# Kernel optimization log

Hardware: AMD Instinct MI355X
Metric: run time of the kernel (lower is better)

## Reference

```python
import jax, jax.numpy as jnp
import numpy as np

D = 1024      # n_embd
H = 16        # n_head
HD = D // H   # head_size = 64


def _layernorm(x, g, b, eps=1e-5):
    mu = jnp.mean(x, axis=-1, keepdims=True)
    var = jnp.mean((x - mu) ** 2, axis=-1, keepdims=True)
    return (x - mu) * jax.lax.rsqrt(var + eps) * g + b


def setup_inputs() -> dict:
    key = jax.random.key(0)
    ks = jax.random.split(key, 12)
    s = lambda fan_in: 1.0 / np.sqrt(fan_in)
    inp = {
        "x": jax.random.normal(ks[0], (4, 2048, D), dtype=jnp.float32),
        # attention projections (bias=False in Head), per-head weights fused into [D, D]
        "wq": jax.random.uniform(ks[1], (D, D), jnp.float32, -s(D), s(D)),
        "wk": jax.random.uniform(ks[2], (D, D), jnp.float32, -s(D), s(D)),
        "wv": jax.random.uniform(ks[3], (D, D), jnp.float32, -s(D), s(D)),
        "wo": jax.random.uniform(ks[4], (D, D), jnp.float32, -s(D), s(D)),
        "bo": jax.random.uniform(ks[5], (D,), jnp.float32, -s(D), s(D)),
        # feed-forward: D -> 4D -> D
        "w1": jax.random.uniform(ks[6], (D, 4 * D), jnp.float32, -s(D), s(D)),
        "b1": jax.random.uniform(ks[7], (4 * D,), jnp.float32, -s(D), s(D)),
        "w2": jax.random.uniform(ks[8], (4 * D, D), jnp.float32, -s(4 * D), s(4 * D)),
        "b2": jax.random.uniform(ks[9], (D,), jnp.float32, -s(4 * D), s(4 * D)),
        # layernorms
        "g_ln1": jnp.ones((D,), jnp.float32),
        "b_ln1": jnp.zeros((D,), jnp.float32),
        "g_ln2": jnp.ones((D,), jnp.float32),
        "b_ln2": jnp.zeros((D,), jnp.float32),
    }
    return inp


def reference(x, wq, wk, wv, wo, bo, w1, b1, w2, b2, g_ln1, b_ln1, g_ln2, b_ln2):
    B, T, _ = x.shape
    # --- self-attention on ln1(x) ---
    h = _layernorm(x, g_ln1, b_ln1)
    q = (h @ wq).reshape(B, T, H, HD)
    k = (h @ wk).reshape(B, T, H, HD)
    v = (h @ wv).reshape(B, T, H, HD)
    scores = jnp.einsum("bqhd,bkhd->bhqk", q, k) * (HD ** -0.5)
    causal = jnp.tril(jnp.ones((T, T), dtype=bool))
    scores = jnp.where(causal, scores, -jnp.inf)
    wei = jax.nn.softmax(scores, axis=-1)                    # [B,H,T,T]
    attn = jnp.einsum("bhqk,bkhd->bqhd", wei, v).reshape(B, T, D)
    x = x + attn @ wo + bo
    # --- feed-forward on ln2(x) ---
    h2 = _layernorm(x, g_ln2, b_ln2)
    x = x + jax.nn.relu(h2 @ w1 + b1) @ w2 + b2
    return x
```

## Files before the change

kernel.cpp:

```cpp
#include <hip/hip_runtime.h>
#include <cstdint>

typedef __bf16 bf16x8 __attribute__((ext_vector_type(8)));
typedef float f32x4 __attribute__((ext_vector_type(4)));
typedef unsigned int u32x4 __attribute__((ext_vector_type(4)));
typedef unsigned int u32x2 __attribute__((ext_vector_type(2)));
typedef unsigned short u16x4 __attribute__((ext_vector_type(4)));

#define D_MODEL 1024
#define SEQ     2048
#define NBATCH  4
#define NHEAD   16
#define HDIM    64
#define NTOK    (NBATCH * SEQ)
#define QSCALE  0.18033688011112042f

__device__ __forceinline__ unsigned short f2bf(float f) {
  unsigned int u = __builtin_bit_cast(unsigned int, f);
  u += 0x7FFFu + ((u >> 16) & 1u);
  return (unsigned short)(u >> 16);
}

__device__ __forceinline__ float bf2f(unsigned short s) {
  return __builtin_bit_cast(float, (unsigned int)s << 16);
}

__device__ __forceinline__ bf16x8 load8bf(const unsigned short* p) {
  return __builtin_bit_cast(bf16x8, *(const u32x4*)p);
}

__device__ __forceinline__ f32x4 mfma16(bf16x8 a, bf16x8 b, f32x4 c) {
  return __builtin_amdgcn_mfma_f32_16x16x32_bf16(a, b, c, 0, 0, 0);
}

__device__ __forceinline__ void gload16(const unsigned short* g, unsigned short* l) {
  __builtin_amdgcn_global_load_lds((__attribute__((address_space(1))) void*)g,
                                   (__attribute__((address_space(3))) void*)l, 16, 0, 0);
}

__global__ __launch_bounds__(256) void tcast_all(const float* __restrict__ wq,
                                                 const float* __restrict__ wk,
                                                 const float* __restrict__ wv,
                                                 const float* __restrict__ wo,
                                                 const float* __restrict__ w1,
                                                 const float* __restrict__ w2,
                                                 unsigned short* __restrict__ wqkv_t,
                                                 unsigned short* __restrict__ wo_t,
                                                 unsigned short* __restrict__ w1_t,
                                                 unsigned short* __restrict__ w2_t) {
  const int id = blockIdx.x;
  const float* in; unsigned short* out; int K, N, k0, n0;
  if (id < 4096) {
    const int seg = id >> 10, r = id & 1023;
    in  = seg == 0 ? wq : seg == 1 ? wk : seg == 2 ? wv : wo;
    out = seg == 3 ? wo_t : wqkv_t + (size_t)seg * 1024 * 1024;
    K = 1024; N = 1024; n0 = (r & 31) * 32; k0 = (r >> 5) * 32;
  } else if (id < 8192) {
    const int r = id - 4096;
    in = w1; out = w1_t; K = 1024; N = 4096;
    n0 = (r & 127) * 32; k0 = (r >> 7) * 32;
  } else {
    const int r = id - 8192;
    in = w2; out = w2_t; K = 4096; N = 1024;
    n0 = (r & 31) * 32; k0 = (r >> 5) * 32;
  }
  __shared__ float tile[32][33];
  const int tx = threadIdx.x & 31, ty = threadIdx.x >> 5;
  #pragma unroll
  for (int j = 0; j < 4; ++j)
    tile[ty + 8 * j][tx] = in[(size_t)(k0 + ty + 8 * j) * N + n0 + tx];
  __syncthreads();
  #pragma unroll
  for (int j = 0; j < 4; ++j)
    out[(size_t)(n0 + ty + 8 * j) * K + k0 + tx] = f2bf(tile[tx][ty + 8 * j]);
}

template <int FPIN>
__global__ __launch_bounds__(256) void ln_kernel(const void* __restrict__ xin,
                                                 const float* __restrict__ g,
                                                 const float* __restrict__ bb,
                                                 unsigned short* __restrict__ out) {
  const int row = blockIdx.x, tid = threadIdx.x;
  float4 xv;
  if (FPIN) {
    xv = ((const float4*)((const float*)xin + (size_t)row * D_MODEL))[tid];
  } else {
    const u16x4 bv4 = ((const u16x4*)((const unsigned short*)xin + (size_t)row * D_MODEL))[tid];
    xv.x = bf2f(bv4.x); xv.y = bf2f(bv4.y); xv.z = bf2f(bv4.z); xv.w = bf2f(bv4.w);
  }
  float s  = xv.x + xv.y + xv.z + xv.w;
  float ss = xv.x * xv.x + xv.y * xv.y + xv.z * xv.z + xv.w * xv.w;
  #pragma unroll
  for (int off = 1; off < 64; off <<= 1) { s += __shfl_xor(s, off); ss += __shfl_xor(ss, off); }
  __shared__ float red[8];
  const int wave = tid >> 6, lane = tid & 63;
  if (lane == 0) { red[wave] = s; red[4 + wave] = ss; }
  __syncthreads();
  s  = red[0] + red[1] + red[2] + red[3];
  ss = red[4] + red[5] + red[6] + red[7];
  const float mu   = s * (1.0f / D_MODEL);
  const float var  = ss * (1.0f / D_MODEL) - mu * mu;
  const float rstd = rsqrtf(var + 1e-5f);
  const float4 gv = ((const float4*)g)[tid];
  const float4 bv = ((const float4*)bb)[tid];
  u16x4 o;
  o.x = f2bf((xv.x - mu) * rstd * gv.x + bv.x);
  o.y = f2bf((xv.y - mu) * rstd * gv.y + bv.y);
  o.z = f2bf((xv.z - mu) * rstd * gv.z + bv.z);
  o.w = f2bf((xv.w - mu) * rstd * gv.w + bv.w);
  *(u16x4*)(out + (size_t)row * D_MODEL + tid * 4) = o;
}

template <bool BIAS, bool RELU, int RES, bool OBF>
__global__ __launch_bounds__(256) void gemm_bt(const unsigned short* __restrict__ A,
                                               const unsigned short* __restrict__ Bt,
                                               const float* __restrict__ bias,
                                               const void* __restrict__ res,
                                               void* __restrict__ out,
                                               int M, int N, int K) {
  __shared__ __align__(16) unsigned short As[128 * 64];
  __shared__ __align__(16) unsigned short Bs[128 * 64];
  const int tid  = threadIdx.x;
  const int lin = blockIdx.y * gridDim.x + blockIdx.x;
  const int xcd = lin & 7, idx = lin >> 3;
  const int by = xcd * 8 + (idx & 7);
  const int bx = idx >> 3;
  const int row0 = by * 128, col0 = bx * 128;
  const int wave = tid >> 6, lane = tid & 63;
  const int wm = wave >> 1, wn = wave & 1;
  const int l15 = lane & 15, quad = lane >> 4;
  f32x4 acc[4][4] = {};

  const int tr = tid >> 3;
  const int tc = (tid & 7) ^ (tr & 7);
  const unsigned short* gA = A  + (size_t)(row0 + tr) * K + tc * 8;
  const unsigned short* gB = Bt + (size_t)(col0 + tr) * K + tc * 8;

  const int rowA = (wm * 64 + l15) * 64;
  const int rowB = (wn * 64 + l15) * 64;
  const int swz0 = (quad ^ (l15 & 7)) * 8;
  const int swz1 = ((4 + quad) ^ (l15 & 7)) * 8;

  for (int k0 = 0; k0 < K; k0 += 64) {
    #pragma unroll
    for (int i = 0; i < 4; ++i) {
      gload16(gA + (size_t)(i * 32) * K + k0, As + (i * 256 + tid) * 8);
      gload16(gB + (size_t)(i * 32) * K + k0, Bs + (i * 256 + tid) * 8);
    }
    __syncthreads();
    #pragma unroll
    for (int kf = 0; kf < 2; ++kf) {
      const int swz = kf ? swz1 : swz0;
      bf16x8 af[4], bfr[4];
      #pragma unroll
      for (int t = 0; t < 4; ++t) {
        af[t]  = load8bf(As + rowA + t * 1024 + swz);
        bfr[t] = load8bf(Bs + rowB + t * 1024 + swz);
      }
      #pragma unroll
      for (int i = 0; i < 4; ++i)
        #pragma unroll
        for (int j = 0; j < 4; ++j)
          acc[i][j] = mfma16(af[i], bfr[j], acc[i][j]);
    }
    __syncthreads();
  }

  const size_t rbase = (size_t)row0 + wm * 64 + quad * 4;
  const int cbase = col0 + wn * 64 + l15;
  #pragma unroll
  for (int i = 0; i < 4; ++i) {
    #pragma unroll
    for (int j = 0; j < 4; ++j) {
      const int col = cbase + j * 16;
      const float bval = BIAS ? bias[col] : 0.0f;
      #pragma unroll
      for (int r = 0; r < 4; ++r) {
        const size_t row = rbase + i * 16 + r;
        float v = acc[i][j][r];
        if (BIAS) v += bval;
        if (RELU) v = fmaxf(v, 0.0f);
        if (RES == 1) v += ((const float*)res)[row * N + col];
        if (RES == 2) v += bf2f(((const unsigned short*)res)[row * N + col]);
        if (OBF)  ((unsigned short*)out)[row * N + col] = f2bf(v);
        else      ((float*)out)[row * N + col] = v;
      }
    }
  }
}

__device__ __forceinline__ void stage_half_512(const unsigned short* __restrict__ src,
                                               unsigned short* dst, int ld, int k0,
                                               int h, int tid) {
  #pragma unroll
  for (int l = 0; l < 2; ++l) {
    const int cid = l * 512 + tid;
    const int r = cid >> 3, p = cid & 7, c = p ^ (r & 7);
    gload16(src + (size_t)(h * 128 + r) * ld + k0 + c * 8, dst + h * 8192 + cid * 8);
  }
}

template <bool BIAS, bool RELU, int RES, bool OBF, bool QKV>
__global__ __launch_bounds__(512, 2) void gemm256(const unsigned short* __restrict__ A,
                                                  const unsigned short* __restrict__ Bt,
                                                  const float* __restrict__ bias,
                                                  const void* __restrict__ res,
                                                  void* __restrict__ out,
                                                  unsigned short* __restrict__ qb,
                                                  unsigned short* __restrict__ kp,
                                                  unsigned short* __restrict__ vt,
                                                  int M, int N, int K) {
  __shared__ __align__(16) unsigned short lds[2][32768];
  const int tid = threadIdx.x;
  const int lin = blockIdx.y * gridDim.x + blockIdx.x;
  const int xcd = lin & 7, idx = lin >> 3;
  const int by = xcd * 4 + (idx & 3);
  const int bx = idx >> 2;
  const int row0 = by * 256, col0 = bx * 256;
  const int wave = tid >> 6, lane = tid & 63;
  const int wm = wave >> 2, wn = wave & 3;
  const int l15 = lane & 15, quad = lane >> 4;
  const int swz0 = (quad ^ (l15 & 7)) * 8;
  const int swz1 = ((4 + quad) ^ (l15 & 7)) * 8;

  const unsigned short* gA = A  + (size_t)row0 * K;
  const unsigned short* gB = Bt + (size_t)col0 * K;

  unsigned short* As0 = &lds[0][0];
  unsigned short* Bs0 = &lds[0][16384];
  unsigned short* As1 = &lds[1][0];
  unsigned short* Bs1 = &lds[1][16384];

  f32x4 acc[8][4] = {};
  const int KT = K >> 6;

  stage_half_512(gA, As0, K, 0, 0, tid);
  stage_half_512(gA, As0, K, 0, 1, tid);
  stage_half_512(gB, Bs0, K, 0, 0, tid);
  stage_half_512(gB, Bs0, K, 0, 1, tid);
  if (KT > 1) {
    stage_half_512(gB, Bs1, K, 64, 0, tid);
    stage_half_512(gB, Bs1, K, 64, 1, tid);
    asm volatile("s_waitcnt vmcnt(4)" ::: "memory");
  } else {
    asm volatile("s_waitcnt vmcnt(0)" ::: "memory");
  }
  asm volatile("s_barrier" ::: "memory");

  for (int t = 0; t < KT; ++t) {
    unsigned short* As  = (t & 1) ? As1 : As0;
    unsigned short* Bs  = (t & 1) ? Bs1 : Bs0;
    unsigned short* Asn = (t & 1) ? As0 : As1;
    const int k1 = (t + 1) << 6, k2 = (t + 2) << 6;
    bf16x8 a0[2][4], b01[2][2], b23[2][2];

    #pragma unroll
    for (int i = 0; i < 4; ++i) {
      const unsigned short* ap = As + (wm * 128 + i * 16 + l15) * 64;
      a0[0][i] = load8bf(ap + swz0);
      a0[1][i] = load8bf(ap + swz1);
    }
    #pragma unroll
    for (int j = 0; j < 2; ++j) {
      const unsigned short* bp = Bs + (wn * 64 + j * 16 + l15) * 64;
      b01[0][j] = load8bf(bp + swz0);
      b01[1][j] = load8bf(bp + swz1);
      const unsigned short* bp2 = Bs + (wn * 64 + 32 + j * 16 + l15) * 64;
      b23[0][j] = load8bf(bp2 + swz0);
      b23[1][j] = load8bf(bp2 + swz1);
    }
    if (t + 1 < KT) {
      stage_half_512(gA, Asn, K, k1, 0, tid);
      stage_half_512(gA, Asn, K, k1, 1, tid);
    }
    __builtin_amdgcn_s_setprio(1);
    #pragma unroll
    for (int kf = 0; kf < 2; ++kf)
      #pragma unroll
      for (int i = 0; i < 4; ++i)
        #pragma unroll
        for (int j = 0; j < 2; ++j)
          acc[i][j] = mfma16(a0[kf][i], b01[kf][j], acc[i][j]);
    #pragma unroll
    for (int kf = 0; kf < 2; ++kf)
      #pragma unroll
      for (int i = 0; i < 4; ++i)
        #pragma unroll
        for (int j = 0; j < 2; ++j)
          acc[i][2 + j] = mfma16(a0[kf][i], b23[kf][j], acc[i][2 + j]);
    __builtin_amdgcn_s_setprio(0);
    __builtin_amdgcn_sched_barrier(0);
    asm volatile("s_barrier" ::: "memory");

    #pragma unroll
    for (int i = 0; i < 4; ++i) {
      const unsigned short* ap = As + (wm * 128 + 64 + i * 16 + l15) * 64;
      a0[0][i] = load8bf(ap + swz0);
      a0[1][i] = load8bf(ap + swz1);
    }
    if (t + 2 < KT) {
      stage_half_512(gB, Bs, K, k2, 0, tid);
      stage_half_512(gB, Bs, K, k2, 1, tid);
    }
    __builtin_amdgcn_s_setprio(1);
    #pragma unroll
    for (int kf = 0; kf < 2; ++kf)
      #pragma unroll
      for (int i = 0; i < 4; ++i)
        #pragma unroll
        for (int j = 0; j < 2; ++j)
          acc[4 + i][2 + j] = mfma16(a0[kf][i], b23[kf][j], acc[4 + i][2 + j]);
    #pragma unroll
    for (int kf = 0; kf < 2; ++kf)
      #pragma unroll
      for (int i = 0; i < 4; ++i)
        #pragma unroll
        for (int j = 0; j < 2; ++j)
          acc[4 + i][j] = mfma16(a0[kf][i], b01[kf][j], acc[4 + i][j]);
    __builtin_amdgcn_s_setprio(0);
    __builtin_amdgcn_sched_barrier(0);
    if (t + 2 < KT) asm volatile("s_waitcnt vmcnt(4)" ::: "memory");
    else            asm volatile("s_waitcnt vmcnt(0)" ::: "memory");
    asm volatile("s_barrier" ::: "memory");
  }

  const size_t rbase = (size_t)row0 + wm * 128 + quad * 4;
  const int cbase = col0 + wn * 64 + l15;
  if (QKV) {
    const int sec = col0 >> 10;
    #pragma unroll
    for (int i = 0; i < 8; ++i) {
      #pragma unroll
      for (int j = 0; j < 4; ++j) {
        const int col = cbase + j * 16;
        if (sec == 0) {
          #pragma unroll
          for (int r = 0; r < 4; ++r) {
            const size_t row = rbase + i * 16 + r;
            qb[row * 1024 + col] = f2bf(acc[i][j][r] * QSCALE);
          }
        } else if (sec == 1) {
          const int c2 = col - 1024, hh = c2 >> 6, d = c2 & 63;
          #pragma unroll
          for (int r = 0; r < 4; ++r) {
            const size_t row = rbase + i * 16 + r;
            const int bb = (int)(row >> 11), tt = (int)(row & 2047);
            kp[(((size_t)(bb * 16 + hh)) * SEQ + tt) * 64 + d] = f2bf(acc[i][j][r]);
          }
        } else {
          const int c2 = col - 2048, hh = c2 >> 6, d = c2 & 63;
          const size_t t0 = rbase + i * 16;
          const int bb = (int)(t0 >> 11);
          u16x4 pk;
          #pragma unroll
          for (int r = 0; r < 4; ++r) pk[r] = f2bf(acc[i][j][r]);
          *(u16x4*)(vt + ((size_t)(bb * 16 + hh) * 64 + d) * SEQ + (t0 & 2047)) = pk;
        }
      }
    }
  } else {
    #pragma unroll
    for (int i = 0; i < 8; ++i) {
      #pragma unroll
      for (int j = 0; j < 4; ++j) {
        const int col = cbase + j * 16;
        const float bval = BIAS ? bias[col] : 0.0f;
        #pragma unroll
        for (int r = 0; r < 4; ++r) {
          const size_t row = rbase + i * 16 + r;
          float v = acc[i][j][r];
          if (BIAS) v += bval;
          if (RELU) v = fmaxf(v, 0.0f);
          if (RES == 1) v += ((const float*)res)[row * N + col];
          if (RES == 2) v += bf2f(((const unsigned short*)res)[row * N + col]);
          if (OBF)  ((unsigned short*)out)[row * N + col] = f2bf(v);
          else      ((float*)out)[row * N + col] = v;
        }
      }
    }
  }
  (void)M;
}

__device__ __forceinline__ void stage32g(const unsigned short* __restrict__ src,
                                         unsigned short* dst, int ld, int k0,
                                         int h128, int t256) {
  #pragma unroll
  for (int l = 0; l < 2; ++l) {
    const int cid = l * 256 + t256;
    const int L = cid >> 3;
    const int p = cid & 7;
    const int c = p ^ (L & 7);
    const int row = h128 * 128 + L * 2 + (c >> 2);
    gload16(src + (size_t)row * ld + k0 + (c & 3) * 8, dst + h128 * 4096 + cid * 8);
  }
}

__device__ __forceinline__ bf16x8 frag32(const unsigned short* tile, int r0,
                                         int l15, int quad) {
  const int row = r0 + l15;
  const int L = row >> 1;
  const int p = ((row & 1) * 4 + quad) ^ (L & 7);
  return load8bf(tile + L * 64 + p * 8);
}

__global__ __launch_bounds__(512, 2) void gemm_ffn2(const unsigned short* __restrict__ A,
                                                    const unsigned short* __restrict__ Bt,
                                                    const float* __restrict__ bias,
                                                    const unsigned short* __restrict__ res,
                                                    float* __restrict__ out) {
  __shared__ __align__(16) unsigned short lds[2][2][12288];
  const int tid = threadIdx.x;
  const int lin = blockIdx.y * gridDim.x + blockIdx.x;
  const int xcd = lin & 7, idx = lin >> 3;
  const int by = xcd * 4 + (idx & 3);
  const int bx = idx >> 2;
  const int row0 = by * 256, col0 = bx * 128;
  const int wave = tid >> 6, lane = tid & 63;
  const int ks = wave >> 2;
  const int w4 = wave & 3;
  const int wm = w4 >> 1, wn = w4 & 1;
  const int l15 = lane & 15, quad = lane >> 4;
  const int t256 = tid & 255;

  const unsigned short* gA = A  + (size_t)row0 * 4096 + ks * 2048;
  const unsigned short* gB = Bt + (size_t)col0 * 4096 + ks * 2048;

  unsigned short* As0 = &lds[ks][0][0];
  unsigned short* Bs0 = &lds[ks][0][8192];
  unsigned short* As1 = &lds[ks][1][0];
  unsigned short* Bs1 = &lds[ks][1][8192];

  f32x4 acc[8][4] = {};
  const int KT = 64;

  stage32g(gA, As0, 4096, 0, 0, t256);
  stage32g(gA, As0, 4096, 0, 1, t256);
  stage32g(gB, Bs0, 4096, 0, 0, t256);
  stage32g(gB, Bs1, 4096, 32, 0, t256);
  asm volatile("s_waitcnt vmcnt(2)" ::: "memory");
  asm volatile("s_barrier" ::: "memory");

  for (int t = 0; t < KT; ++t) {
    unsigned short* As  = (t & 1) ? As1 : As0;
    unsigned short* Bs  = (t & 1) ? Bs1 : Bs0;
    unsigned short* Asn = (t & 1) ? As0 : As1;
    const int k1 = (t + 1) << 5, k2 = (t + 2) << 5;
    bf16x8 a[4], b[4];

    #pragma unroll
    for (int j = 0; j < 4; ++j) b[j] = frag32(Bs, wn * 64 + j * 16, l15, quad);
    #pragma unroll
    for (int i = 0; i < 4; ++i) a[i] = frag32(As, wm * 128 + i * 16, l15, quad);
    if (t + 1 < KT) {
      stage32g(gA, Asn, 4096, k1, 0, t256);
      stage32g(gA, Asn, 4096, k1, 1, t256);
    }
    __builtin_amdgcn_s_setprio(1);
    #pragma unroll
    for (int i = 0; i < 4; ++i)
      #pragma unroll
      for (int j = 0; j < 4; ++j)
        acc[i][j] = mfma16(a[i], b[j], acc[i][j]);
    __builtin_amdgcn_s_setprio(0);
    __builtin_amdgcn_sched_barrier(0);
    asm volatile("s_barrier" ::: "memory");

    #pragma unroll
    for (int i = 0; i < 4; ++i) a[i] = frag32(As, wm * 128 + 64 + i * 16, l15, quad);
    if (t + 2 < KT) stage32g(gB, Bs, 4096, k2, 0, t256);
    __builtin_amdgcn_s_setprio(1);
    #pragma unroll
    for (int i = 0; i < 4; ++i)
      #pragma unroll
      for (int j = 0; j < 4; ++j)
        acc[4 + i][j] = mfma16(a[i], b[j], acc[4 + i][j]);
    __builtin_amdgcn_s_setprio(0);
    __builtin_amdgcn_sched_barrier(0);
    if (t + 2 < KT) asm volatile("s_waitcnt vmcnt(2)" ::: "memory");
    else            asm volatile("s_waitcnt vmcnt(0)" ::: "memory");
    asm volatile("s_barrier" ::: "memory");
  }

  float* ex = (float*)&lds[0][0][0];
  #pragma unroll
  for (int half = 0; half < 2; ++half) {
    __syncthreads();
    if (ks == 1) {
      #pragma unroll
      for (int i = 0; i < 4; ++i)
        #pragma unroll
        for (int j = 0; j < 4; ++j)
          *(f32x4*)(ex + ((size_t)(w4 * 16 + i * 4 + j)) * 256 + lane * 4) =
              acc[half * 4 + i][j];
    }
    __syncthreads();
    if (ks == 0) {
      #pragma unroll
      for (int i = 0; i < 4; ++i)
        #pragma unroll
        for (int j = 0; j < 4; ++j) {
          const f32x4 v = *(const f32x4*)(ex + ((size_t)(w4 * 16 + i * 4 + j)) * 256 + lane * 4);
          acc[half * 4 + i][j] += v;
        }
    }
  }
  if (ks == 0) {
    const size_t rbase = (size_t)row0 + wm * 128 + quad * 4;
    const int cbase = col0 + wn * 64 + l15;
    #pragma unroll
    for (int i = 0; i < 8; ++i) {
      #pragma unroll
      for (int j = 0; j < 4; ++j) {
        const int col = cbase + j * 16;
        const float bval = bias[col];
        #pragma unroll
        for (int r = 0; r < 4; ++r) {
          const size_t row = rbase + i * 16 + r;
          out[row * 1024 + col] = acc[i][j][r] + bval + bf2f(res[row * 1024 + col]);
        }
      }
    }
  }
}

__global__ __launch_bounds__(256) void attn5(const unsigned short* __restrict__ qb,
                                             const unsigned short* __restrict__ kp,
                                             const unsigned short* __restrict__ vt,
                                             unsigned short* __restrict__ attnb) {
  const int lin = (blockIdx.z * 16 + blockIdx.y) * 8 + blockIdx.x;
  const int xcd = lin & 7, idx = lin >> 3;
  const int bh = xcd * 8 + (idx >> 3);
  const int xb = idx & 7;
  const int b = bh >> 4, h = bh & 15;
  const int tid = threadIdx.x, wave = tid >> 6, lane = tid & 63;
  const int l15 = lane & 15, quad = lane >> 4;
  const size_t tokbase = (size_t)b * SEQ;

  __shared__ __align__(16) unsigned short ks[64 * 64];
  __shared__ __align__(16) unsigned short vts[64 * 64];
  __shared__ __align__(16) unsigned short plds[4][32 * 64];

  const unsigned short* kbase = kp + (size_t)bh * SEQ * HDIM;
  const unsigned short* vbase = vt + (size_t)bh * HDIM * SEQ;

  for (int half = 0; half < 2; ++half) {
    const int qblk = (half == 0) ? (15 - xb) : xb;
    const int qw0 = qblk * 128 + wave * 32;

    bf16x8 qf[2][2];
    #pragma unroll
    for (int qfi = 0; qfi < 2; ++qfi)
      #pragma unroll
      for (int kf = 0; kf < 2; ++kf)
        qf[qfi][kf] = load8bf(qb + (tokbase + qw0 + qfi * 16 + l15) * 1024
                              + h * HDIM + kf * 32 + quad * 8);

    f32x4 o[2][4] = {};
    float lsum[2] = {0.0f, 0.0f};

    const int ntiles = qblk * 2 + 2;
    for (int kt = 0; kt < ntiles; ++kt) {
      const int k0 = kt * 64;
      __syncthreads();
      #pragma unroll
      for (int i = 0; i < 2; ++i) {
        const int cid = i * 256 + tid;
        const int r = cid >> 3, p = cid & 7, c = p ^ (r & 7);
        gload16(kbase + (size_t)(k0 + r) * HDIM + c * 8, ks + cid * 8);
      }
      #pragma unroll
      for (int i = 0; i < 2; ++i) {
        const int cid = i * 256 + tid;
        const int d = cid >> 3, p = cid & 7, c = p ^ (d & 7);
        gload16(vbase + (size_t)d * SEQ + k0 + c * 8, vts + cid * 8);
      }
      __syncthreads();
      if (k0 <= qw0 + 31) {
        f32x4 s[4][2] = {};
        #pragma unroll
        for (int kf = 0; kf < 2; ++kf)
          #pragma unroll
          for (int keyf = 0; keyf < 4; ++keyf) {
            const int row = keyf * 16 + l15;
            const int p = (kf * 4 + quad) ^ (row & 7);
            const bf16x8 kfr = load8bf(ks + row * 64 + p * 8);
            s[keyf][0] = mfma16(kfr, qf[0][kf], s[keyf][0]);
            s[keyf][1] = mfma16(kfr, qf[1][kf], s[keyf][1]);
          }
        #pragma unroll
        for (int qfi = 0; qfi < 2; ++qfi) {
          const int q = qw0 + qfi * 16 + l15;
          const int qloc = qfi * 16 + l15;
          #pragma unroll
          for (int keyf = 0; keyf < 4; ++keyf) {
            unsigned int pw[4];
            #pragma unroll
            for (int r = 0; r < 4; ++r) {
              const int key = k0 + keyf * 16 + quad * 4 + r;
              float p = __builtin_amdgcn_exp2f(s[keyf][qfi][r]);
              p = (key > q) ? 0.0f : p;
              pw[r] = __builtin_bit_cast(unsigned int, p);
              lsum[qfi] += __builtin_bit_cast(float, pw[r] & 0xFFFF0000u);
            }
            u32x2 packed;
            packed.x = (pw[0] >> 16) | (pw[1] & 0xFFFF0000u);
            packed.y = (pw[2] >> 16) | (pw[3] & 0xFFFF0000u);
            const int slot = (keyf * 4 + quad) ^ ((l15 & 7) << 1);
            *(u32x2*)(&plds[wave][qloc * 64 + slot * 4]) = packed;
          }
        }
        __builtin_amdgcn_s_waitcnt(0);
        #pragma unroll
        for (int kf = 0; kf < 2; ++kf) {
          bf16x8 pa[2];
          #pragma unroll
          for (int mf = 0; mf < 2; ++mf) {
            const int lq = mf * 16 + l15;
            const int c = (kf * 4 + quad) ^ (l15 & 7);
            pa[mf] = load8bf(&plds[wave][lq * 64 + c * 8]);
          }
          #pragma unroll
          for (int df = 0; df < 4; ++df) {
            const int row = df * 16 + l15;
            const int p = (kf * 4 + quad) ^ (row & 7);
            const bf16x8 vb = load8bf(vts + row * 64 + p * 8);
            o[0][df] = mfma16(pa[0], vb, o[0][df]);
            o[1][df] = mfma16(pa[1], vb, o[1][df]);
          }
        }
      }
    }
    #pragma unroll
    for (int mf = 0; mf < 2; ++mf) {
      float l = lsum[mf];
      l += __shfl_xor(l, 16);
      l += __shfl_xor(l, 32);
      const float rl = 1.0f / l;
      #pragma unroll
      for (int r = 0; r < 4; ++r) {
        const float rv = __shfl(rl, quad * 4 + r);
        const size_t row = tokbase + qw0 + mf * 16 + quad * 4 + r;
        #pragma unroll
        for (int df = 0; df < 4; ++df)
          attnb[row * D_MODEL + h * HDIM + df * 16 + l15] = f2bf(o[mf][df][r] * rv);
      }
    }
  }
}

extern "C" void kernel_launch(void* const* d_in, const int* in_sizes, int n_in,
                              void* d_out, int out_size, void* d_ws, size_t ws_size,
                              hipStream_t stream) {
  const float* x    = (const float*)d_in[0];
  const float* wq   = (const float*)d_in[1];
  const float* wk   = (const float*)d_in[2];
  const float* wv   = (const float*)d_in[3];
  const float* wo   = (const float*)d_in[4];
  const float* bo   = (const float*)d_in[5];
  const float* w1   = (const float*)d_in[6];
  const float* b1   = (const float*)d_in[7];
  const float* w2   = (const float*)d_in[8];
  const float* b2   = (const float*)d_in[9];
  const float* g1   = (const float*)d_in[10];
  const float* bl1  = (const float*)d_in[11];
  const float* g2   = (const float*)d_in[12];
  const float* bl2  = (const float*)d_in[13];
  float* out = (float*)d_out;

  char* ws = (char*)d_ws;
  size_t off = 0;
  auto alloc = [&](size_t bytes) { char* p = ws + off; off += (bytes + 255) & ~(size_t)255; return p; };
  unsigned short* wqkv_t = (unsigned short*)alloc((size_t)3072 * 1024 * 2);
  unsigned short* wo_t   = (unsigned short*)alloc((size_t)1024 * 1024 * 2);
  unsigned short* w1_t   = (unsigned short*)alloc((size_t)4096 * 1024 * 2);
  unsigned short* w2_t   = (unsigned short*)alloc((size_t)1024 * 4096 * 2);
  unsigned short* h1     = (unsigned short*)alloc((size_t)NTOK * 1024 * 2);
  unsigned short* kpb    = (unsigned short*)alloc((size_t)NTOK * 1024 * 2);
  unsigned short* vtb    = (unsigned short*)alloc((size_t)NTOK * 1024 * 2);
  unsigned short* attnb  = (unsigned short*)alloc((size_t)NTOK * 1024 * 2);
  unsigned short* h2     = (unsigned short*)alloc((size_t)NTOK * 1024 * 2);
  unsigned short* ffn1   = (unsigned short*)alloc((size_t)NTOK * 4096 * 2);
  unsigned short* qb  = attnb;
  unsigned short* x1b = h1;

  tcast_all<<<12288, 256, 0, stream>>>(wq, wk, wv, wo, w1, w2,
                                       wqkv_t, wo_t, w1_t, w2_t);
  ln_kernel<1><<<NTOK, 256, 0, stream>>>(x, g1, bl1, h1);
  gemm256<false, false, 0, true, true><<<dim3(12, 32), 512, 0, stream>>>(
      h1, wqkv_t, nullptr, nullptr, nullptr, qb, kpb, vtb, NTOK, 3072, 1024);
  attn5<<<dim3(SEQ / 256, NHEAD, NBATCH), 256, 0, stream>>>(qb, kpb, vtb, attnb);
  gemm_bt<true, false, 1, true><<<dim3(8, 64), 256, 0, stream>>>(
      attnb, wo_t, bo, x, x1b, NTOK, 1024, 1024);
  ln_kernel<0><<<NTOK, 256, 0, stream>>>(x1b, g2, bl2, h2);
  gemm256<true, true, 0, true, false><<<dim3(16, 32), 512, 0, stream>>>(
      h2, w1_t, b1, nullptr, ffn1, nullptr, nullptr, nullptr, NTOK, 4096, 1024);
  gemm_ffn2<<<dim3(8, 32), 512, 0, stream>>>(ffn1, w2_t, b2, x1b, out);
  (void)in_sizes; (void)n_in; (void)out_size; (void)ws_size;
}
```

Baseline: 447.3 us.

## Double-buffer K/V tiles in attention kernel to overlap loads with compute

The attention kernel now uses two shared-memory buffers for the K and V^T tiles. It issues the global-to-LDS loads for tile kt+1 before computing on tile kt, which replaces the two barriers per iteration with a single wait-plus-barrier at the end of each iteration. This is meant to hide global memory latency behind the MFMA and softmax work. The LDS wait before the P·V stage is narrowed to lgkmcnt only, so outstanding prefetch loads are not drained there. The cost is doubled LDS for K/V, which may reduce occupancy, and the added scheduling barriers constrain how the compiler can interleave instructions.

```diff
diff --git a/kernel.cpp b/kernel.cpp
--- a/kernel.cpp
+++ b/kernel.cpp
@@ -537,8 +537,8 @@
   const int l15 = lane & 15, quad = lane >> 4;
   const size_t tokbase = (size_t)b * SEQ;
 
-  __shared__ __align__(16) unsigned short ks[64 * 64];
-  __shared__ __align__(16) unsigned short vts[64 * 64];
+  __shared__ __align__(16) unsigned short ks[2][64 * 64];
+  __shared__ __align__(16) unsigned short vts[2][64 * 64];
   __shared__ __align__(16) unsigned short plds[4][32 * 64];
 
   const unsigned short* kbase = kp + (size_t)bh * SEQ * HDIM;
@@ -560,23 +560,45 @@
     float lsum[2] = {0.0f, 0.0f};
 
     const int ntiles = qblk * 2 + 2;
-    for (int kt = 0; kt < ntiles; ++kt) {
-      const int k0 = kt * 64;
-      __syncthreads();
+
+    {
       #pragma unroll
       for (int i = 0; i < 2; ++i) {
         const int cid = i * 256 + tid;
         const int r = cid >> 3, p = cid & 7, c = p ^ (r & 7);
-        gload16(kbase + (size_t)(k0 + r) * HDIM + c * 8, ks + cid * 8);
+        gload16(kbase + (size_t)r * HDIM + c * 8, &ks[0][cid * 8]);
       }
       #pragma unroll
       for (int i = 0; i < 2; ++i) {
         const int cid = i * 256 + tid;
         const int d = cid >> 3, p = cid & 7, c = p ^ (d & 7);
-        gload16(vbase + (size_t)d * SEQ + k0 + c * 8, vts + cid * 8);
-      }
-      __syncthreads();
+        gload16(vbase + (size_t)d * SEQ + c * 8, &vts[0][cid * 8]);
+      }
+      asm volatile("s_waitcnt vmcnt(0)" ::: "memory");
+      asm volatile("s_barrier" ::: "memory");
+    }
+
+    for (int kt = 0; kt < ntiles; ++kt) {
+      const int k0 = kt * 64;
+      if (kt + 1 < ntiles) {
+        const int kn = (kt + 1) * 64;
+        const int nb = (kt + 1) & 1;
+        #pragma unroll
+        for (int i = 0; i < 2; ++i) {
+          const int cid = i * 256 + tid;
+          const int r = cid >> 3, p = cid & 7, c = p ^ (r & 7);
+          gload16(kbase + (size_t)(kn + r) * HDIM + c * 8, &ks[nb][cid * 8]);
+        }
+        #pragma unroll
+        for (int i = 0; i < 2; ++i) {
+          const int cid = i * 256 + tid;
+          const int d = cid >> 3, p = cid & 7, c = p ^ (d & 7);
+          gload16(vbase + (size_t)d * SEQ + kn + c * 8, &vts[nb][cid * 8]);
+        }
+      }
       if (k0 <= qw0 + 31) {
+        const unsigned short* ksb  = ks[kt & 1];
+        const unsigned short* vtsb = vts[kt & 1];
         f32x4 s[4][2] = {};
         #pragma unroll
         for (int kf = 0; kf < 2; ++kf)
@@ -584,7 +606,7 @@
           for (int keyf = 0; keyf < 4; ++keyf) {
             const int row = keyf * 16 + l15;
             const int p = (kf * 4 + quad) ^ (row & 7);
-            const bf16x8 kfr = load8bf(ks + row * 64 + p * 8);
+            const bf16x8 kfr = load8bf(ksb + row * 64 + p * 8);
             s[keyf][0] = mfma16(kfr, qf[0][kf], s[keyf][0]);
             s[keyf][1] = mfma16(kfr, qf[1][kf], s[keyf][1]);
           }
@@ -610,7 +632,8 @@
             *(u32x2*)(&plds[wave][qloc * 64 + slot * 4]) = packed;
           }
         }
-        __builtin_amdgcn_s_waitcnt(0);
+        asm volatile("s_waitcnt lgkmcnt(0)" ::: "memory");
+        __builtin_amdgcn_sched_barrier(0);
         #pragma unroll
         for (int kf = 0; kf < 2; ++kf) {
           bf16x8 pa[2];
@@ -624,12 +647,15 @@
           for (int df = 0; df < 4; ++df) {
             const int row = df * 16 + l15;
             const int p = (kf * 4 + quad) ^ (row & 7);
-            const bf16x8 vb = load8bf(vts + row * 64 + p * 8);
+            const bf16x8 vb = load8bf(vtsb + row * 64 + p * 8);
             o[0][df] = mfma16(pa[0], vb, o[0][df]);
             o[1][df] = mfma16(pa[1], vb, o[1][df]);
           }
         }
       }
+      __builtin_amdgcn_sched_barrier(0);
+      asm volatile("s_waitcnt vmcnt(0)" ::: "memory");
+      asm volatile("s_barrier" ::: "memory");
     }
     #pragma unroll
     for (int mf = 0; mf < 2; ++mf) {
```

After: 445.6 us. About the same (-0.4%).
